# Performance work log

Measured on AMD Instinct MI355X. Metric: run time of the kernel, lower is better.

## Reference

```python
import jax, jax.numpy as jnp
import numpy as np

N_NODES = 100000
N_EDGES = 1600000
F_IN, HIDDEN, N_CLS = 128, 128, 40


def _gcn_layer(h, W, b, src, dst, norm, n):
    # h: [n, d_in] -> linear transform then edge-normalized scatter-add
    h = h @ W                                   # [n, d_out]
    msg = h[src] * norm[:, None]                # gather over edges [E', d_out]
    out = jax.ops.segment_sum(msg, dst, num_segments=n)
    return out + b


def setup_inputs() -> dict:
    key = jax.random.key(0)
    k1, k2, k3, k4 = jax.random.split(key, 4)
    x = jax.random.normal(k1, (N_NODES, F_IN), dtype=jnp.float32)
    edge_index = jax.random.randint(k2, (2, N_EDGES), 0, N_NODES, dtype=jnp.int32)
    # glorot-style init
    W1 = jax.random.normal(k3, (F_IN, HIDDEN), dtype=jnp.float32) * (1.0 / np.sqrt(F_IN))
    W2 = jax.random.normal(k4, (HIDDEN, N_CLS), dtype=jnp.float32) * (1.0 / np.sqrt(HIDDEN))
    b1 = jnp.zeros((HIDDEN,), dtype=jnp.float32)
    b2 = jnp.zeros((N_CLS,), dtype=jnp.float32)
    return {"x": x, "edge_index": edge_index, "W1": W1, "b1": b1,
            "W2": W2, "b2": b2, "dropout": 0}


def reference(x, edge_index, W1, b1, W2, b2, dropout):
    n = x.shape[0]
    src, dst = edge_index[0], edge_index[1]
    # add self loops (PyG GCNConv default)
    loop = jnp.arange(n, dtype=src.dtype)
    src = jnp.concatenate([src, loop])
    dst = jnp.concatenate([dst, loop])
    # symmetric normalization D^{-1/2} (A+I) D^{-1/2}
    deg = jax.ops.segment_sum(jnp.ones(src.shape, dtype=x.dtype), dst, num_segments=n)
    dinv = jnp.where(deg > 0, jax.lax.rsqrt(deg), 0.0)
    norm = dinv[src] * dinv[dst]                # [E + n]
    h = jax.nn.relu(_gcn_layer(x, W1, b1, src, dst, norm, n))
    # F.dropout with training=False is identity (eval mode)
    return _gcn_layer(h, W2, b2, src, dst, norm, n)
```

## Files before the change

### kernel.cpp

```cpp
#include <hip/hip_runtime.h>
#include <stdint.h>


#define NF 128
#define NC 40
#define PSHIFT 7
#define PNODES 128
#define GH 256

typedef __attribute__((ext_vector_type(8))) short short8;
typedef __attribute__((ext_vector_type(4))) float float4m;

__device__ __forceinline__ float bflo2f(unsigned int u) {
  union { unsigned int i; float f; } v; v.i = u << 16; return v.f;
}
__device__ __forceinline__ float bfhi2f(unsigned int u) {
  union { unsigned int i; float f; } v; v.i = u & 0xffff0000u; return v.f;
}
__device__ __forceinline__ unsigned short f2bf(float f) {
  union { float f; unsigned int i; } v; v.f = f;
  unsigned int x = v.i;
  return (unsigned short)((x + 0x7fffu + ((x >> 16) & 1u)) >> 16);
}

__global__ __launch_bounds__(256) void pack_k(const float* __restrict__ W1,
                                              unsigned short* __restrict__ Bpack) {
  int frag = blockIdx.x * 256 + threadIdx.x;
  int ct = frag >> 8, ks = (frag >> 6) & 3, lane = frag & 63;
  int quad = lane >> 4, l15 = lane & 15;
  int col = ct * 16 + l15, krow = ks * 32 + quad * 8;
  ushort4 lo, hi;
  lo.x = f2bf(W1[(krow + 0) * 128 + col]);
  lo.y = f2bf(W1[(krow + 1) * 128 + col]);
  lo.z = f2bf(W1[(krow + 2) * 128 + col]);
  lo.w = f2bf(W1[(krow + 3) * 128 + col]);
  hi.x = f2bf(W1[(krow + 4) * 128 + col]);
  hi.y = f2bf(W1[(krow + 5) * 128 + col]);
  hi.z = f2bf(W1[(krow + 6) * 128 + col]);
  hi.w = f2bf(W1[(krow + 7) * 128 + col]);
  *(ushort4*)&Bpack[(size_t)frag * 8 + 0] = lo;
  *(ushort4*)&Bpack[(size_t)frag * 8 + 4] = hi;
}

__global__ __launch_bounds__(256) void hist_k(const int* __restrict__ ei,
                                              int* __restrict__ histT,
                                              int E, int CPB, int NPART) {
  __shared__ int h[1024];
  int tid = threadIdx.x, bid = blockIdx.x;
  for (int i = tid; i < NPART; i += 256) h[i] = 0;
  __syncthreads();
  int e0 = bid * CPB, e1 = min(e0 + CPB, E);
  for (int e = e0 + tid; e < e1; e += 256)
    atomicAdd(&h[ei[E + e] >> PSHIFT], 1);
  __syncthreads();
  for (int i = tid; i < NPART; i += 256) histT[(size_t)i * GH + bid] = h[i];
}

__global__ __launch_bounds__(256) void scanA_k(int* __restrict__ histT,
                                               int* __restrict__ partTotal) {
  __shared__ int sm[GH];
  int tid = threadIdx.x, p = blockIdx.x;
  int v = histT[(size_t)p * GH + tid];
  sm[tid] = v; __syncthreads();
  for (int off = 1; off < GH; off <<= 1) {
    int t = (tid >= off) ? sm[tid - off] : 0;
    __syncthreads();
    sm[tid] += t;
    __syncthreads();
  }
  histT[(size_t)p * GH + tid] = sm[tid] - v;
  if (tid == GH - 1) partTotal[p] = sm[GH - 1];
}

__global__ __launch_bounds__(1024) void scanB_k(const int* __restrict__ partTotal,
                                                int* __restrict__ base, int NPART) {
  __shared__ int sm[1024];
  int tid = threadIdx.x;
  int v = (tid < NPART) ? partTotal[tid] : 0;
  sm[tid] = v; __syncthreads();
  for (int off = 1; off < 1024; off <<= 1) {
    int t = (tid >= off) ? sm[tid - off] : 0;
    __syncthreads();
    sm[tid] += t;
    __syncthreads();
  }
  if (tid < NPART) base[tid] = sm[tid] - v;
}

__global__ __launch_bounds__(256) void scatter_k(const int* __restrict__ ei,
                                                 const int* __restrict__ histT,
                                                 const int* __restrict__ base,
                                                 unsigned int* __restrict__ epart,
                                                 int E, int CPB, int NPART) {
  __shared__ int off[1024];
  int tid = threadIdx.x, bid = blockIdx.x;
  for (int i = tid; i < NPART; i += 256)
    off[i] = base[i] + histT[(size_t)i * GH + bid];
  __syncthreads();
  int e0 = bid * CPB, e1 = min(e0 + CPB, E);
  for (int e = e0 + tid; e < e1; e += 256) {
    int s = ei[e], d = ei[E + e];
    int pos = atomicAdd(&off[d >> PSHIFT], 1);
    epart[pos] = ((unsigned int)(d & (PNODES - 1)) << 25) | (unsigned int)s;
  }
}

__global__ __launch_bounds__(256) void build_gemm_k(
    const float* __restrict__ x, const unsigned short* __restrict__ Bpack,
    unsigned short* __restrict__ Hs, const unsigned int* __restrict__ epart,
    const int* __restrict__ base, const int* __restrict__ partTotal,
    int* __restrict__ cnt, float* __restrict__ dinv,
    int* __restrict__ bucket, int n, int NPART, int G1) {
  __shared__ alignas(16) char smem[50176];
  int tid = threadIdx.x, bid = blockIdx.x;

  if (bid % 3 == 2) {
    int pidx = bid / 3;
    if (pidx >= NPART) return;
    int* lcnt = (int*)smem;
    int* lbuck = lcnt + PNODES;
    if (tid < PNODES) lcnt[tid] = 0;
    __syncthreads();
    int st = base[pidx], m = partTotal[pidx];
    for (int e = tid; e < m; e += 256) {
      unsigned int u = epart[(size_t)st + e];
      int ln = (int)(u >> 25), s = (int)(u & 0x1ffffffu);
      int pos = atomicAdd(&lcnt[ln], 1);
      if (pos < 64) lbuck[ln * 64 + pos] = s;
    }
    __syncthreads();
    int node0 = pidx << PSHIFT;
    int nn = min(PNODES, n - node0);
    int4* bg = (int4*)&bucket[(size_t)node0 * 64];
    const int4* bl = (const int4*)lbuck;
    for (int i = tid; i < nn * 16; i += 256) bg[i] = bl[i];
    if (tid < nn) {
      int c = lcnt[tid];
      cnt[node0 + tid] = c;
      dinv[node0 + tid] = rsqrtf((float)c + 1.0f);
    }
    return;
  }

  int idx = (bid / 3) * 2 + (bid % 3);
  if (idx >= G1) return;
  unsigned short* As = (unsigned short*)smem;
  unsigned short* Bs = (unsigned short*)(smem + 17408);
  int r0 = idx * 64;

  const float4* x4 = (const float4*)x;
  for (int i = tid; i < 2048; i += 256) {
    int kc = i & 31, r = i >> 5;
    float4 v = make_float4(0.f, 0.f, 0.f, 0.f);
    if (r0 + r < n) v = x4[(size_t)(r0 + r) * 32 + kc];
    ushort4 o;
    o.x = f2bf(v.x); o.y = f2bf(v.y); o.z = f2bf(v.z); o.w = f2bf(v.w);
    *(ushort4*)&As[r * 136 + kc * 4] = o;
  }
  {
    const uint4* bp4 = (const uint4*)Bpack;
    uint4* bs4 = (uint4*)Bs;
    for (int i = tid; i < 2048; i += 256) bs4[i] = bp4[i];
  }
  __syncthreads();

  int wv = tid >> 6, lane = tid & 63;
  int quad = lane >> 4, l15 = lane & 15;

  short8 afr[4];
#pragma unroll
  for (int ks = 0; ks < 4; ks++)
    afr[ks] = *(const short8*)&As[(wv * 16 + l15) * 136 + ks * 32 + quad * 8];

  float4m acc[8];
#pragma unroll
  for (int i = 0; i < 8; i++) acc[i] = (float4m){0.f, 0.f, 0.f, 0.f};

#pragma unroll
  for (int ct = 0; ct < 8; ct++) {
#pragma unroll
    for (int ks = 0; ks < 4; ks++) {
      short8 bfr = *(const short8*)&Bs[(((ct * 4 + ks) * 64) + lane) * 8];
      acc[ct] = __builtin_amdgcn_mfma_f32_16x16x32_bf16(afr[ks], bfr, acc[ct], 0, 0, 0);
    }
  }

  int rbase = r0 + wv * 16 + quad * 4;
#pragma unroll
  for (int ct = 0; ct < 8; ct++) {
#pragma unroll
    for (int reg = 0; reg < 4; reg++) {
      int r = rbase + reg;
      if (r < n) Hs[(size_t)r * 128 + ct * 16 + l15] = f2bf(acc[ct][reg]);
    }
  }
}

__global__ __launch_bounds__(256) void agg1_k(const unsigned int* __restrict__ Hs2,
                                              const int* __restrict__ cnt,
                                              const int* __restrict__ bucket,
                                              const float* __restrict__ dinv,
                                              const float2* __restrict__ b1v,
                                              unsigned int* __restrict__ out1, int n) {
  int gw = (blockIdx.x * 256 + threadIdx.x) >> 6;
  if (gw >= n) return;
  int lane = threadIdx.x & 63;

  float d = dinv[gw];
  unsigned int v = Hs2[(size_t)gw * 64 + lane];
  float a0 = d * bflo2f(v), a1 = d * bfhi2f(v);

  int m = cnt[gw]; if (m > 64) m = 64;
  const int* bp = &bucket[(size_t)gw * 64];
  int p = 0;
  for (; p + 7 < m; p += 8) {
    int j0 = bp[p], j1 = bp[p+1], j2 = bp[p+2], j3 = bp[p+3];
    int j4 = bp[p+4], j5 = bp[p+5], j6 = bp[p+6], j7 = bp[p+7];
    float d0 = dinv[j0], d1 = dinv[j1], d2 = dinv[j2], d3 = dinv[j3];
    float d4 = dinv[j4], d5 = dinv[j5], d6 = dinv[j6], d7 = dinv[j7];
    unsigned int u0 = Hs2[(size_t)j0 * 64 + lane];
    unsigned int u1 = Hs2[(size_t)j1 * 64 + lane];
    unsigned int u2 = Hs2[(size_t)j2 * 64 + lane];
    unsigned int u3 = Hs2[(size_t)j3 * 64 + lane];
    unsigned int u4 = Hs2[(size_t)j4 * 64 + lane];
    unsigned int u5 = Hs2[(size_t)j5 * 64 + lane];
    unsigned int u6 = Hs2[(size_t)j6 * 64 + lane];
    unsigned int u7 = Hs2[(size_t)j7 * 64 + lane];
    a0 += d0 * bflo2f(u0) + d1 * bflo2f(u1) + d2 * bflo2f(u2) + d3 * bflo2f(u3)
        + d4 * bflo2f(u4) + d5 * bflo2f(u5) + d6 * bflo2f(u6) + d7 * bflo2f(u7);
    a1 += d0 * bfhi2f(u0) + d1 * bfhi2f(u1) + d2 * bfhi2f(u2) + d3 * bfhi2f(u3)
        + d4 * bfhi2f(u4) + d5 * bfhi2f(u5) + d6 * bfhi2f(u6) + d7 * bfhi2f(u7);
  }
  for (; p + 3 < m; p += 4) {
    int j0 = bp[p], j1 = bp[p+1], j2 = bp[p+2], j3 = bp[p+3];
    float d0 = dinv[j0], d1 = dinv[j1], d2 = dinv[j2], d3 = dinv[j3];
    unsigned int u0 = Hs2[(size_t)j0 * 64 + lane];
    unsigned int u1 = Hs2[(size_t)j1 * 64 + lane];
    unsigned int u2 = Hs2[(size_t)j2 * 64 + lane];
    unsigned int u3 = Hs2[(size_t)j3 * 64 + lane];
    a0 += d0 * bflo2f(u0) + d1 * bflo2f(u1) + d2 * bflo2f(u2) + d3 * bflo2f(u3);
    a1 += d0 * bfhi2f(u0) + d1 * bfhi2f(u1) + d2 * bfhi2f(u2) + d3 * bfhi2f(u3);
  }
  for (; p < m; p++) {
    int j = bp[p];
    float dj = dinv[j];
    unsigned int u = Hs2[(size_t)j * 64 + lane];
    a0 += dj * bflo2f(u); a1 += dj * bfhi2f(u);
  }

  float2 bv = b1v[lane];
  float r0 = fmaxf(0.0f, bv.x + d * a0);
  float r1 = fmaxf(0.0f, bv.y + d * a1);
  out1[(size_t)gw * 64 + lane] =
      (unsigned int)f2bf(r0) | ((unsigned int)f2bf(r1) << 16);
}

__global__ __launch_bounds__(320) void gemm2_k(const unsigned short* __restrict__ h,
                                               const float* __restrict__ W2,
                                               const float* __restrict__ dinv,
                                               unsigned short* __restrict__ H2s, int n) {
  __shared__ unsigned short xsT[128 * 136];
  __shared__ float W2s[128 * 48];
  int tid = threadIdx.x;
  int r0 = blockIdx.x * 128;

  const float4* w4 = (const float4*)W2;
  for (int i = tid; i < 1280; i += 320) {
    int k = i / 10, q = i - k * 10;
    *(float4*)&W2s[k * 48 + q * 4] = w4[i];
  }

  const uint4* x4 = (const uint4*)h;
  for (int i = tid; i < 2048; i += 320) {
    int r = i & 127, kc = i >> 7;
    uint4 v = make_uint4(0u, 0u, 0u, 0u);
    if (r0 + r < n) v = x4[(size_t)(r0 + r) * 16 + kc];
    int kb = kc * 8;
    xsT[(kb + 0) * 136 + r] = (unsigned short)(v.x & 0xffffu);
    xsT[(kb + 1) * 136 + r] = (unsigned short)(v.x >> 16);
    xsT[(kb + 2) * 136 + r] = (unsigned short)(v.y & 0xffffu);
    xsT[(kb + 3) * 136 + r] = (unsigned short)(v.y >> 16);
    xsT[(kb + 4) * 136 + r] = (unsigned short)(v.z & 0xffffu);
    xsT[(kb + 5) * 136 + r] = (unsigned short)(v.z >> 16);
    xsT[(kb + 6) * 136 + r] = (unsigned short)(v.w & 0xffffu);
    xsT[(kb + 7) * 136 + r] = (unsigned short)(v.w >> 16);
  }
  __syncthreads();

  int rg = tid & 31, cg = tid >> 5;
  int rb = rg * 4, c0 = cg * 4;
  float acc[4][4] = {};
#pragma unroll 4
  for (int k = 0; k < 128; k++) {
    uint2 xv = *(const uint2*)&xsT[k * 136 + rb];
    float x0 = bflo2f(xv.x), x1 = bfhi2f(xv.x);
    float x2 = bflo2f(xv.y), x3 = bfhi2f(xv.y);
    float4 wv = *(const float4*)&W2s[k * 48 + c0];
    acc[0][0] += x0 * wv.x; acc[0][1] += x0 * wv.y; acc[0][2] += x0 * wv.z; acc[0][3] += x0 * wv.w;
    acc[1][0] += x1 * wv.x; acc[1][1] += x1 * wv.y; acc[1][2] += x1 * wv.z; acc[1][3] += x1 * wv.w;
    acc[2][0] += x2 * wv.x; acc[2][1] += x2 * wv.y; acc[2][2] += x2 * wv.z; acc[2][3] += x2 * wv.w;
    acc[3][0] += x3 * wv.x; acc[3][1] += x3 * wv.y; acc[3][2] += x3 * wv.z; acc[3][3] += x3 * wv.w;
  }

#pragma unroll
  for (int i = 0; i < 4; i++) {
    int r = r0 + rb + i;
    if (r < n) {
      float dd = dinv[r];
      ushort4 o;
      o.x = f2bf(acc[i][0] * dd); o.y = f2bf(acc[i][1] * dd);
      o.z = f2bf(acc[i][2] * dd); o.w = f2bf(acc[i][3] * dd);
      *(ushort4*)&H2s[(size_t)r * 40 + c0] = o;
    }
  }
}

__global__ __launch_bounds__(256) void agg2_k(const unsigned int* __restrict__ H2u,
                                              const int* __restrict__ cnt,
                                              const int* __restrict__ bucket,
                                              const float* __restrict__ dinv,
                                              const float* __restrict__ b2,
                                              float* __restrict__ outp, int n) {
  int w = (blockIdx.x * 256 + threadIdx.x) >> 6;
  int lane = threadIdx.x & 63;
  int sub = lane / 20, ci = lane - sub * 20;
  int node = w * 3 + sub;
  if (sub >= 3 || node >= n) return;

  float d = dinv[node];
  unsigned int u = H2u[(size_t)node * 20 + ci];
  float a0 = bflo2f(u), a1 = bfhi2f(u);

  int m = cnt[node]; if (m > 64) m = 64;
  const int* bp = &bucket[(size_t)node * 64];
  int p = 0;
  for (; p + 3 < m; p += 4) {
    int j0 = bp[p], j1 = bp[p+1], j2 = bp[p+2], j3 = bp[p+3];
    unsigned int u0 = H2u[(size_t)j0 * 20 + ci];
    unsigned int u1 = H2u[(size_t)j1 * 20 + ci];
    unsigned int u2 = H2u[(size_t)j2 * 20 + ci];
    unsigned int u3 = H2u[(size_t)j3 * 20 + ci];
    a0 += bflo2f(u0) + bflo2f(u1) + bflo2f(u2) + bflo2f(u3);
    a1 += bfhi2f(u0) + bfhi2f(u1) + bfhi2f(u2) + bfhi2f(u3);
  }
  for (; p < m; p++) {
    unsigned int uu = H2u[(size_t)bp[p] * 20 + ci];
    a0 += bflo2f(uu); a1 += bfhi2f(uu);
  }

  float2 o;
  o.x = b2[2 * ci]     + d * a0;
  o.y = b2[2 * ci + 1] + d * a1;
  *(float2*)&outp[(size_t)node * 40 + 2 * ci] = o;
}

extern "C" void kernel_launch(void* const* d_in, const int* in_sizes, int n_in,
                              void* d_out, int out_size, void* d_ws, size_t ws_size,
                              hipStream_t stream) {
  const float* x  = (const float*)d_in[0];
  const int*   ei = (const int*)d_in[1];
  const float* W1 = (const float*)d_in[2];
  const float* b1 = (const float*)d_in[3];
  const float* W2 = (const float*)d_in[4];
  const float* b2 = (const float*)d_in[5];

  int N = in_sizes[0] / NF;
  int E = in_sizes[1] / 2;
  int NPART = (N + PNODES - 1) >> PSHIFT;
  int CPB = (E + GH - 1) / GH;
  int G1 = (N + 63) / 64;

  char* ws = (char*)d_ws;
  size_t off = 0;
  auto carve = [&](size_t bytes) {
    void* p = ws + off;
    off += (bytes + 255) & ~(size_t)255;
    return p;
  };
  int*            cnt       = (int*)carve((size_t)N * 4);
  float*          dinv      = (float*)carve((size_t)N * 4);
  int*            bucket    = (int*)carve((size_t)N * 64 * 4);
  unsigned short* Hs        = (unsigned short*)carve((size_t)N * NF * 2);
  unsigned short* out1      = (unsigned short*)carve((size_t)N * NF * 2);
  int*            histT     = (int*)carve((size_t)NPART * GH * 4);
  int*            partTotal = (int*)carve((size_t)NPART * 4);
  int*            base      = (int*)carve((size_t)NPART * 4);
  unsigned int*   epart     = (unsigned int*)carve((size_t)E * 4);
  unsigned short* Bpack     = (unsigned short*)carve(16384 * 2);
  unsigned short* H2s       = Hs;

  pack_k<<<8, 256, 0, stream>>>(W1, Bpack);
  hist_k<<<GH, 256, 0, stream>>>(ei, histT, E, CPB, NPART);
  scanA_k<<<NPART, 256, 0, stream>>>(histT, partTotal);
  scanB_k<<<1, 1024, 0, stream>>>(partTotal, base, NPART);
  scatter_k<<<GH, 256, 0, stream>>>(ei, histT, base, epart, E, CPB, NPART);
  build_gemm_k<<<3 * NPART, 256, 0, stream>>>(x, Bpack, Hs, epart, base, partTotal,
                                              cnt, dinv, bucket, N, NPART, G1);
  agg1_k<<<((size_t)N * 64 + 255) / 256, 256, 0, stream>>>((const unsigned int*)Hs,
                                                           cnt, bucket, dinv,
                                                           (const float2*)b1,
                                                           (unsigned int*)out1, N);
  gemm2_k<<<(N + 127) / 128, 320, 0, stream>>>(out1, W2, dinv, H2s, N);
  int NW = (N + 2) / 3;
  agg2_k<<<((size_t)NW * 64 + 255) / 256, 256, 0, stream>>>((const unsigned int*)H2s,
                                                            cnt, bucket, dinv, b2,
                                                            (float*)d_out, N);
}
```

Measured before the change: 297.4 us.

## Fuse layer-1 aggregation with layer-2 GEMM via MFMA and merge weight packing

Layer-1 aggregation now keeps its 16-row bf16 output tile in shared memory and immediately multiplies it by a prepacked bf16 W2 with MFMA. This removes the out1 round trip through global memory and one kernel launch. W1 and W2 packing also move into extra blocks of the histogram kernel, dropping the separate pack launch. The cost is that each block now handles only 16 nodes, 4 per wave in sequence, which may reduce latency hiding in the gather. W2 also becomes bf16 where the old GEMM used fp32 weights.

```diff
diff --git a/kernel.cpp b/kernel.cpp
--- a/kernel.cpp
+++ b/kernel.cpp
@@ -23,30 +23,36 @@
   return (unsigned short)((x + 0x7fffu + ((x >> 16) & 1u)) >> 16);
 }
 
-__global__ __launch_bounds__(256) void pack_k(const float* __restrict__ W1,
-                                              unsigned short* __restrict__ Bpack) {
-  int frag = blockIdx.x * 256 + threadIdx.x;
-  int ct = frag >> 8, ks = (frag >> 6) & 3, lane = frag & 63;
-  int quad = lane >> 4, l15 = lane & 15;
-  int col = ct * 16 + l15, krow = ks * 32 + quad * 8;
-  ushort4 lo, hi;
-  lo.x = f2bf(W1[(krow + 0) * 128 + col]);
-  lo.y = f2bf(W1[(krow + 1) * 128 + col]);
-  lo.z = f2bf(W1[(krow + 2) * 128 + col]);
-  lo.w = f2bf(W1[(krow + 3) * 128 + col]);
-  hi.x = f2bf(W1[(krow + 4) * 128 + col]);
-  hi.y = f2bf(W1[(krow + 5) * 128 + col]);
-  hi.z = f2bf(W1[(krow + 6) * 128 + col]);
-  hi.w = f2bf(W1[(krow + 7) * 128 + col]);
-  *(ushort4*)&Bpack[(size_t)frag * 8 + 0] = lo;
-  *(ushort4*)&Bpack[(size_t)frag * 8 + 4] = hi;
-}
-
-__global__ __launch_bounds__(256) void hist_k(const int* __restrict__ ei,
-                                              int* __restrict__ histT,
-                                              int E, int CPB, int NPART) {
+__global__ __launch_bounds__(256) void hist_pack_k(
+    const int* __restrict__ ei, int* __restrict__ histT, int E, int CPB, int NPART,
+    const float* __restrict__ W1, const float* __restrict__ W2,
+    unsigned short* __restrict__ Bpack, unsigned short* __restrict__ W2pack) {
+  int tid = threadIdx.x, bid = blockIdx.x;
+  if (bid >= GH) {
+    int g = (bid - GH) * 256 + tid;
+    const float* W; unsigned short* dst; int cols, frag;
+    if (g < 2048)      { W = W1; dst = Bpack;  cols = 128; frag = g; }
+    else if (g < 2816) { W = W2; dst = W2pack; cols = 40;  frag = g - 2048; }
+    else return;
+    int ct = frag >> 8, ks = (frag >> 6) & 3, lane = frag & 63;
+    int quad = lane >> 4, l15 = lane & 15;
+    int col = ct * 16 + l15, krow = ks * 32 + quad * 8;
+    ushort4 lo = {0,0,0,0}, hi = {0,0,0,0};
+    if (col < cols) {
+      lo.x = f2bf(W[(krow + 0) * cols + col]);
+      lo.y = f2bf(W[(krow + 1) * cols + col]);
+      lo.z = f2bf(W[(krow + 2) * cols + col]);
+      lo.w = f2bf(W[(krow + 3) * cols + col]);
+      hi.x = f2bf(W[(krow + 4) * cols + col]);
+      hi.y = f2bf(W[(krow + 5) * cols + col]);
+      hi.z = f2bf(W[(krow + 6) * cols + col]);
+      hi.w = f2bf(W[(krow + 7) * cols + col]);
+    }
+    *(ushort4*)&dst[(size_t)frag * 8 + 0] = lo;
+    *(ushort4*)&dst[(size_t)frag * 8 + 4] = hi;
+    return;
+  }
   __shared__ int h[1024];
-  int tid = threadIdx.x, bid = blockIdx.x;
   for (int i = tid; i < NPART; i += 256) h[i] = 0;
   __syncthreads();
   int e0 = bid * CPB, e1 = min(e0 + CPB, E);
@@ -196,121 +202,97 @@
   }
 }
 
-__global__ __launch_bounds__(256) void agg1_k(const unsigned int* __restrict__ Hs2,
-                                              const int* __restrict__ cnt,
-                                              const int* __restrict__ bucket,
-                                              const float* __restrict__ dinv,
-                                              const float2* __restrict__ b1v,
-                                              unsigned int* __restrict__ out1, int n) {
-  int gw = (blockIdx.x * 256 + threadIdx.x) >> 6;
-  if (gw >= n) return;
-  int lane = threadIdx.x & 63;
-
-  float d = dinv[gw];
-  unsigned int v = Hs2[(size_t)gw * 64 + lane];
-  float a0 = d * bflo2f(v), a1 = d * bfhi2f(v);
-
-  int m = cnt[gw]; if (m > 64) m = 64;
-  const int* bp = &bucket[(size_t)gw * 64];
-  int p = 0;
-  for (; p + 7 < m; p += 8) {
-    int j0 = bp[p], j1 = bp[p+1], j2 = bp[p+2], j3 = bp[p+3];
-    int j4 = bp[p+4], j5 = bp[p+5], j6 = bp[p+6], j7 = bp[p+7];
-    float d0 = dinv[j0], d1 = dinv[j1], d2 = dinv[j2], d3 = dinv[j3];
-    float d4 = dinv[j4], d5 = dinv[j5], d6 = dinv[j6], d7 = dinv[j7];
-    unsigned int u0 = Hs2[(size_t)j0 * 64 + lane];
-    unsigned int u1 = Hs2[(size_t)j1 * 64 + lane];
-    unsigned int u2 = Hs2[(size_t)j2 * 64 + lane];
-    unsigned int u3 = Hs2[(size_t)j3 * 64 + lane];
-    unsigned int u4 = Hs2[(size_t)j4 * 64 + lane];
-    unsigned int u5 = Hs2[(size_t)j5 * 64 + lane];
-    unsigned int u6 = Hs2[(size_t)j6 * 64 + lane];
-    unsigned int u7 = Hs2[(size_t)j7 * 64 + lane];
-    a0 += d0 * bflo2f(u0) + d1 * bflo2f(u1) + d2 * bflo2f(u2) + d3 * bflo2f(u3)
-        + d4 * bflo2f(u4) + d5 * bflo2f(u5) + d6 * bflo2f(u6) + d7 * bflo2f(u7);
-    a1 += d0 * bfhi2f(u0) + d1 * bfhi2f(u1) + d2 * bfhi2f(u2) + d3 * bfhi2f(u3)
-        + d4 * bfhi2f(u4) + d5 * bfhi2f(u5) + d6 * bfhi2f(u6) + d7 * bfhi2f(u7);
-  }
-  for (; p + 3 < m; p += 4) {
-    int j0 = bp[p], j1 = bp[p+1], j2 = bp[p+2], j3 = bp[p+3];
-    float d0 = dinv[j0], d1 = dinv[j1], d2 = dinv[j2], d3 = dinv[j3];
-    unsigned int u0 = Hs2[(size_t)j0 * 64 + lane];
-    unsigned int u1 = Hs2[(size_t)j1 * 64 + lane];
-    unsigned int u2 = Hs2[(size_t)j2 * 64 + lane];
-    unsigned int u3 = Hs2[(size_t)j3 * 64 + lane];
-    a0 += d0 * bflo2f(u0) + d1 * bflo2f(u1) + d2 * bflo2f(u2) + d3 * bflo2f(u3);
-    a1 += d0 * bfhi2f(u0) + d1 * bfhi2f(u1) + d2 * bfhi2f(u2) + d3 * bfhi2f(u3);
-  }
-  for (; p < m; p++) {
-    int j = bp[p];
-    float dj = dinv[j];
-    unsigned int u = Hs2[(size_t)j * 64 + lane];
-    a0 += dj * bflo2f(u); a1 += dj * bfhi2f(u);
-  }
-
-  float2 bv = b1v[lane];
-  float r0 = fmaxf(0.0f, bv.x + d * a0);
-  float r1 = fmaxf(0.0f, bv.y + d * a1);
-  out1[(size_t)gw * 64 + lane] =
-      (unsigned int)f2bf(r0) | ((unsigned int)f2bf(r1) << 16);
-}
-
-__global__ __launch_bounds__(320) void gemm2_k(const unsigned short* __restrict__ h,
-                                               const float* __restrict__ W2,
+__global__ __launch_bounds__(256) void agg1f_k(const unsigned int* __restrict__ Hs2,
+                                               const int* __restrict__ cnt,
+                                               const int* __restrict__ bucket,
                                                const float* __restrict__ dinv,
+                                               const float2* __restrict__ b1v,
+                                               const unsigned short* __restrict__ W2pack,
                                                unsigned short* __restrict__ H2s, int n) {
-  __shared__ unsigned short xsT[128 * 136];
-  __shared__ float W2s[128 * 48];
-  int tid = threadIdx.x;
-  int r0 = blockIdx.x * 128;
-
-  const float4* w4 = (const float4*)W2;
-  for (int i = tid; i < 1280; i += 320) {
-    int k = i / 10, q = i - k * 10;
-    *(float4*)&W2s[k * 48 + q * 4] = w4[i];
-  }
-
-  const uint4* x4 = (const uint4*)h;
-  for (int i = tid; i < 2048; i += 320) {
-    int r = i & 127, kc = i >> 7;
-    uint4 v = make_uint4(0u, 0u, 0u, 0u);
-    if (r0 + r < n) v = x4[(size_t)(r0 + r) * 16 + kc];
-    int kb = kc * 8;
-    xsT[(kb + 0) * 136 + r] = (unsigned short)(v.x & 0xffffu);
-    xsT[(kb + 1) * 136 + r] = (unsigned short)(v.x >> 16);
-    xsT[(kb + 2) * 136 + r] = (unsigned short)(v.y & 0xffffu);
-    xsT[(kb + 3) * 136 + r] = (unsigned short)(v.y >> 16);
-    xsT[(kb + 4) * 136 + r] = (unsigned short)(v.z & 0xffffu);
-    xsT[(kb + 5) * 136 + r] = (unsigned short)(v.z >> 16);
-    xsT[(kb + 6) * 136 + r] = (unsigned short)(v.w & 0xffffu);
-    xsT[(kb + 7) * 136 + r] = (unsigned short)(v.w >> 16);
-  }
-  __syncthreads();
-
-  int rg = tid & 31, cg = tid >> 5;
-  int rb = rg * 4, c0 = cg * 4;
-  float acc[4][4] = {};
-#pragma unroll 4
-  for (int k = 0; k < 128; k++) {
-    uint2 xv = *(const uint2*)&xsT[k * 136 + rb];
-    float x0 = bflo2f(xv.x), x1 = bfhi2f(xv.x);
-    float x2 = bflo2f(xv.y), x3 = bfhi2f(xv.y);
-    float4 wv = *(const float4*)&W2s[k * 48 + c0];
-    acc[0][0] += x0 * wv.x; acc[0][1] += x0 * wv.y; acc[0][2] += x0 * wv.z; acc[0][3] += x0 * wv.w;
-    acc[1][0] += x1 * wv.x; acc[1][1] += x1 * wv.y; acc[1][2] += x1 * wv.z; acc[1][3] += x1 * wv.w;
-    acc[2][0] += x2 * wv.x; acc[2][1] += x2 * wv.y; acc[2][2] += x2 * wv.z; acc[2][3] += x2 * wv.w;
-    acc[3][0] += x3 * wv.x; acc[3][1] += x3 * wv.y; acc[3][2] += x3 * wv.z; acc[3][3] += x3 * wv.w;
-  }
-
-#pragma unroll
-  for (int i = 0; i < 4; i++) {
-    int r = r0 + rb + i;
-    if (r < n) {
-      float dd = dinv[r];
-      ushort4 o;
-      o.x = f2bf(acc[i][0] * dd); o.y = f2bf(acc[i][1] * dd);
-      o.z = f2bf(acc[i][2] * dd); o.w = f2bf(acc[i][3] * dd);
-      *(ushort4*)&H2s[(size_t)r * 40 + c0] = o;
+  __shared__ unsigned short As[16 * 136];
+  __shared__ unsigned short W2s[768 * 8];
+  int tid = threadIdx.x, wv = tid >> 6, lane = tid & 63;
+  int node0 = blockIdx.x * 16;
+
+  {
+    const uint4* p = (const uint4*)W2pack;
+    uint4* q = (uint4*)W2s;
+    for (int i = tid; i < 768; i += 256) q[i] = p[i];
+  }
+
+  for (int s = 0; s < 4; s++) {
+    int mrow = wv * 4 + s;
+    int node = node0 + mrow;
+    float r0 = 0.f, r1 = 0.f;
+    if (node < n) {
+      float d = dinv[node];
+      unsigned int v = Hs2[(size_t)node * 64 + lane];
+      float a0 = d * bflo2f(v), a1 = d * bfhi2f(v);
+      int m = cnt[node]; if (m > 64) m = 64;
+      const int* bp = &bucket[(size_t)node * 64];
+      int p = 0;
+      for (; p + 7 < m; p += 8) {
+        int j0 = bp[p], j1 = bp[p+1], j2 = bp[p+2], j3 = bp[p+3];
+        int j4 = bp[p+4], j5 = bp[p+5], j6 = bp[p+6], j7 = bp[p+7];
+        float d0 = dinv[j0], d1 = dinv[j1], d2 = dinv[j2], d3 = dinv[j3];
+        float d4 = dinv[j4], d5 = dinv[j5], d6 = dinv[j6], d7 = dinv[j7];
+        unsigned int u0 = Hs2[(size_t)j0 * 64 + lane];
+        unsigned int u1 = Hs2[(size_t)j1 * 64 + lane];
+        unsigned int u2 = Hs2[(size_t)j2 * 64 + lane];
+        unsigned int u3 = Hs2[(size_t)j3 * 64 + lane];
+        unsigned int u4 = Hs2[(size_t)j4 * 64 + lane];
+        unsigned int u5 = Hs2[(size_t)j5 * 64 + lane];
+        unsigned int u6 = Hs2[(size_t)j6 * 64 + lane];
+        unsigned int u7 = Hs2[(size_t)j7 * 64 + lane];
+        a0 += d0 * bflo2f(u0) + d1 * bflo2f(u1) + d2 * bflo2f(u2) + d3 * bflo2f(u3)
+            + d4 * bflo2f(u4) + d5 * bflo2f(u5) + d6 * bflo2f(u6) + d7 * bflo2f(u7);
+        a1 += d0 * bfhi2f(u0) + d1 * bfhi2f(u1) + d2 * bfhi2f(u2) + d3 * bfhi2f(u3)
+            + d4 * bfhi2f(u4) + d5 * bfhi2f(u5) + d6 * bfhi2f(u6) + d7 * bfhi2f(u7);
+      }
+      for (; p + 3 < m; p += 4) {
+        int j0 = bp[p], j1 = bp[p+1], j2 = bp[p+2], j3 = bp[p+3];
+        float d0 = dinv[j0], d1 = dinv[j1], d2 = dinv[j2], d3 = dinv[j3];
+        unsigned int u0 = Hs2[(size_t)j0 * 64 + lane];
+        unsigned int u1 = Hs2[(size_t)j1 * 64 + lane];
+        unsigned int u2 = Hs2[(size_t)j2 * 64 + lane];
+        unsigned int u3 = Hs2[(size_t)j3 * 64 + lane];
+        a0 += d0 * bflo2f(u0) + d1 * bflo2f(u1) + d2 * bflo2f(u2) + d3 * bflo2f(u3);
+        a1 += d0 * bfhi2f(u0) + d1 * bfhi2f(u1) + d2 * bfhi2f(u2) + d3 * bfhi2f(u3);
+      }
+      for (; p < m; p++) {
+        int j = bp[p];
+        float dj = dinv[j];
+        unsigned int u = Hs2[(size_t)j * 64 + lane];
+        a0 += dj * bflo2f(u); a1 += dj * bfhi2f(u);
+      }
+      float2 bv = b1v[lane];
+      r0 = fmaxf(0.0f, bv.x + d * a0);
+      r1 = fmaxf(0.0f, bv.y + d * a1);
+    }
+    unsigned int pk = (unsigned int)f2bf(r0) | ((unsigned int)f2bf(r1) << 16);
+    *(unsigned int*)&As[mrow * 136 + lane * 2] = pk;
+  }
+  __syncthreads();
+
+  if (wv < 3) {
+    int quad = lane >> 4, l15 = lane & 15;
+    float4m acc = (float4m){0.f, 0.f, 0.f, 0.f};
+#pragma unroll
+    for (int ks = 0; ks < 4; ks++) {
+      short8 afr = *(const short8*)&As[l15 * 136 + ks * 32 + quad * 8];
+      short8 bfr = *(const short8*)&W2s[(((wv * 4 + ks) * 64) + lane) * 8];
+      acc = __builtin_amdgcn_mfma_f32_16x16x32_bf16(afr, bfr, acc, 0, 0, 0);
+    }
+    int c = wv * 16 + l15;
+    if (c < NC) {
+#pragma unroll
+      for (int reg = 0; reg < 4; reg++) {
+        int node = node0 + quad * 4 + reg;
+        if (node < n) {
+          float dd = dinv[node];
+          H2s[(size_t)node * 40 + c] = f2bf(acc[reg] * dd);
+        }
+      }
     }
   }
 }
@@ -381,26 +363,23 @@
   float*          dinv      = (float*)carve((size_t)N * 4);
   int*            bucket    = (int*)carve((size_t)N * 64 * 4);
   unsigned short* Hs        = (unsigned short*)carve((size_t)N * NF * 2);
-  unsigned short* out1      = (unsigned short*)carve((size_t)N * NF * 2);
   int*            histT     = (int*)carve((size_t)NPART * GH * 4);
   int*            partTotal = (int*)carve((size_t)NPART * 4);
   int*            base      = (int*)carve((size_t)NPART * 4);
   unsigned int*   epart     = (unsigned int*)carve((size_t)E * 4);
-  unsigned short* Bpack     = (unsigned short*)carve(16384 * 2);
-  unsigned short* H2s       = Hs;
-
-  pack_k<<<8, 256, 0, stream>>>(W1, Bpack);
-  hist_k<<<GH, 256, 0, stream>>>(ei, histT, E, CPB, NPART);
+  unsigned short* Bpack     = (unsigned short*)carve(2048 * 8 * 2);
+  unsigned short* W2pack    = (unsigned short*)carve(768 * 8 * 2);
+  unsigned short* H2s       = (unsigned short*)carve((size_t)N * NC * 2);
+
+  hist_pack_k<<<GH + 11, 256, 0, stream>>>(ei, histT, E, CPB, NPART,
+                                           W1, W2, Bpack, W2pack);
   scanA_k<<<NPART, 256, 0, stream>>>(histT, partTotal);
   scanB_k<<<1, 1024, 0, stream>>>(partTotal, base, NPART);
   scatter_k<<<GH, 256, 0, stream>>>(ei, histT, base, epart, E, CPB, NPART);
   build_gemm_k<<<3 * NPART, 256, 0, stream>>>(x, Bpack, Hs, epart, base, partTotal,
                                               cnt, dinv, bucket, N, NPART, G1);
-  agg1_k<<<((size_t)N * 64 + 255) / 256, 256, 0, stream>>>((const unsigned int*)Hs,
-                                                           cnt, bucket, dinv,
-                                                           (const float2*)b1,
-                                                           (unsigned int*)out1, N);
-  gemm2_k<<<(N + 127) / 128, 320, 0, stream>>>(out1, W2, dinv, H2s, N);
+  agg1f_k<<<(N + 15) / 16, 256, 0, stream>>>((const unsigned int*)Hs, cnt, bucket,
+                                             dinv, (const float2*)b1, W2pack, H2s, N);
   int NW = (N + 2) / 3;
   agg2_k<<<((size_t)NW * 64 + 255) / 256, 256, 0, stream>>>((const unsigned int*)H2s,
                                                             cnt, bucket, dinv, b2,
```

New measurement: 273.6 us. 1.09x faster.
